# Optimization experiments

Measured on AMD Instinct MI355X. Metric: run time of the kernel, lower is better.

Reference implementation:

```python
import jax, jax.numpy as jnp
import numpy as np

N_NODES = 100000
N_EDGES = 1600000
IN_CH, HID_CH, OUT_CH = 128, 256, 128


def _sage_conv(x, src, dst, W_l, b_l, W_r, n_nodes):
    """PyG SAGEConv with mean aggregation: lin_l(mean_j x_j) + lin_r(x)."""
    # gather source features per edge, scatter-sum into destination nodes
    agg = jax.ops.segment_sum(x[src], dst, num_segments=n_nodes)  # [N, C]
    deg = jax.ops.segment_sum(jnp.ones((src.shape[0],), x.dtype), dst,
                              num_segments=n_nodes)               # [N]
    mean = agg / jnp.maximum(deg, 1.0)[:, None]
    return mean @ W_l + b_l + x @ W_r


def setup_inputs() -> dict:
    key = jax.random.key(0)
    ks = jax.random.split(key, 8)
    x = jax.random.normal(ks[0], (N_NODES, IN_CH), dtype=jnp.float32)
    edge_index = jax.random.randint(ks[1], (2, N_EDGES), 0, N_NODES, dtype=jnp.int64)
    s1 = 1.0 / np.sqrt(IN_CH)
    s2 = 1.0 / np.sqrt(HID_CH)
    W1_l = jax.random.normal(ks[2], (IN_CH, HID_CH), dtype=jnp.float32) * s1
    W1_r = jax.random.normal(ks[3], (IN_CH, HID_CH), dtype=jnp.float32) * s1
    b1 = jnp.zeros((HID_CH,), dtype=jnp.float32)
    W2_l = jax.random.normal(ks[4], (HID_CH, OUT_CH), dtype=jnp.float32) * s2
    W2_r = jax.random.normal(ks[5], (HID_CH, OUT_CH), dtype=jnp.float32) * s2
    b2 = jnp.zeros((OUT_CH,), dtype=jnp.float32)
    return {"x": x, "edge_index": edge_index, "W1_l": W1_l, "b1": b1,
            "W1_r": W1_r, "W2_l": W2_l, "b2": b2, "W2_r": W2_r}


def reference(x, edge_index, W1_l, b1, W1_r, W2_l, b2, W2_r):
    src, dst = edge_index[0], edge_index[1]
    h = _sage_conv(x, src, dst, W1_l, b1, W1_r, N_NODES)
    h = jax.nn.relu(h)
    out = _sage_conv(h, src, dst, W2_l, b2, W2_r, N_NODES)
    return out
```

## Files before the change

kernel.cpp:

```cpp
#include <hip/hip_runtime.h>
#include <cstddef>

#define N_NODES_C 100000
#define N_EDGES_C 1600000

#define NPB 64
#define NB 1563
#define SENT_ROW 100000

#define NCB 196
#define K2_EPB 8192
#define K2_BLOCKS 196

#define CONV_BLOCKS 12500
#define WB_BLOCKS 512

typedef unsigned short u16;
typedef __attribute__((ext_vector_type(8))) short bf16x8;
typedef __attribute__((ext_vector_type(4))) float f32x4;

__device__ __forceinline__ u16 f2bf(float f) {
    unsigned u = __float_as_uint(f);
    u += 0x7fffu + ((u >> 16) & 1);
    return (u16)(u >> 16);
}
__device__ __forceinline__ float lo16f(unsigned v) {
    return __uint_as_float(v << 16);
}
__device__ __forceinline__ float hi16f(unsigned v) {
    return __uint_as_float(v & 0xffff0000u);
}


__global__ __launch_bounds__(256) void front_fused(
    const float* __restrict__ x,
    const float* __restrict__ W1l, const float* __restrict__ W1r,
    const float* __restrict__ W2l, const float* __restrict__ W2r,
    u16* __restrict__ x_bf, u16* __restrict__ T1l, u16* __restrict__ T1r,
    u16* __restrict__ T2l, u16* __restrict__ T2r, u16* __restrict__ p2z) {
    const int b = blockIdx.x;
    const int t = threadIdx.x;
    if (b < CONV_BLOCKS) {
        int i = b * 256 + t;
        if (i < 3200000) {
            float4 v = ((const float4*)x)[i];
            ushort4 o;
            o.x = f2bf(v.x); o.y = f2bf(v.y); o.z = f2bf(v.z); o.w = f2bf(v.w);
            ((ushort4*)x_bf)[i] = o;
        }
    } else if (b < CONV_BLOCKS + WB_BLOCKS) {
        int id = (b - CONV_BLOCKS) * 256 + t;
        int which = id >> 15;
        int r = id & 32767;
        if (which == 0) {
            int n = r >> 7, k = r & 127;
            T1l[r] = f2bf(W1l[k * 256 + n]);
        } else if (which == 1) {
            int n = r >> 7, k = r & 127;
            T1r[r] = f2bf(W1r[k * 256 + n]);
        } else if (which == 2) {
            int n = r >> 8, k = r & 255;
            T2l[r] = f2bf(W2l[k * 128 + n]);
        } else {
            int n = r >> 8, k = r & 255;
            T2r[r] = f2bf(W2r[k * 128 + n]);
        }
    } else {
        uint4 z; z.x = 0; z.y = 0; z.z = 0; z.w = 0;
        if (t < 16)
            ((uint4*)(x_bf + (size_t)SENT_ROW * 128))[t] = z;
        else if (t < 32)
            ((uint4*)(p2z + (size_t)SENT_ROW * 128))[t - 16] = z;
    }
}


__global__ __launch_bounds__(1024) void hist196(const int* __restrict__ dst,
                                                int* __restrict__ chist) {
    __shared__ int hist[NCB];
    const int t = threadIdx.x;
    if (t < NCB) hist[t] = 0;
    __syncthreads();
    const int e0 = blockIdx.x * K2_EPB;
#pragma unroll
    for (int r = 0; r < 2; ++r) {
        int i = (e0 >> 2) + r * 1024 + t;
        if (i * 4 < N_EDGES_C) {
            int4 d = ((const int4*)dst)[i];
            atomicAdd(&hist[d.x >> 9], 1);
            atomicAdd(&hist[d.y >> 9], 1);
            atomicAdd(&hist[d.z >> 9], 1);
            atomicAdd(&hist[d.w >> 9], 1);
        }
    }
    __syncthreads();
    if (t < NCB) {
        int c = hist[t];
        if (c) atomicAdd(&chist[t], c);
    }
}


__global__ __launch_bounds__(256) void cscan(const int* __restrict__ chist,
                                             int* __restrict__ cbase,
                                             int* __restrict__ ccursor) {
    __shared__ int s[256];
    int t = threadIdx.x;
    int v = (t < NCB) ? chist[t] : 0;
    s[t] = v;
    __syncthreads();
    for (int off = 1; off < 256; off <<= 1) {
        int u = (t >= off) ? s[t - off] : 0;
        __syncthreads();
        s[t] += u;
        __syncthreads();
    }
    if (t < NCB) {
        int e = s[t] - v;
        cbase[t] = e;
        ccursor[t] = e;
    }
}


__global__ __launch_bounds__(1024) void coarse_scatter(
    const int* __restrict__ src, const int* __restrict__ dst,
    int* __restrict__ ccursor, unsigned* __restrict__ epkt2) {
    __shared__ unsigned spkt[K2_EPB];
    __shared__ unsigned char scb[K2_EPB];
    __shared__ int hist[NCB], lstart[NCB], lcur[NCB], grun[NCB], stmp[NCB];

    const int t = threadIdx.x;
    const int e0 = blockIdx.x * K2_EPB;
    const int cnt = min(K2_EPB, N_EDGES_C - e0);

    if (t < NCB) hist[t] = 0;
    __syncthreads();

    int4 dd[2], ss[2];
    int vi[2];
#pragma unroll
    for (int r = 0; r < 2; ++r) {
        int i = (e0 >> 2) + r * 1024 + t;
        vi[r] = (i * 4 < N_EDGES_C);
        if (vi[r]) {
            dd[r] = ((const int4*)dst)[i];
            ss[r] = ((const int4*)src)[i];
            atomicAdd(&hist[dd[r].x >> 9], 1);
            atomicAdd(&hist[dd[r].y >> 9], 1);
            atomicAdd(&hist[dd[r].z >> 9], 1);
            atomicAdd(&hist[dd[r].w >> 9], 1);
        }
    }
    __syncthreads();

    if (t < NCB) stmp[t] = hist[t];
    __syncthreads();
    for (int off = 1; off < NCB; off <<= 1) {
        int v = 0;
        if (t < NCB && t >= off) v = stmp[t - off];
        __syncthreads();
        if (t < NCB) stmp[t] += v;
        __syncthreads();
    }
    if (t < NCB) {
        int excl = stmp[t] - hist[t];
        lstart[t] = excl;
        lcur[t] = excl;
        if (hist[t]) grun[t] = atomicAdd(&ccursor[t], hist[t]);
    }
    __syncthreads();

#pragma unroll
    for (int r = 0; r < 2; ++r) {
        if (vi[r]) {
            int4 d = dd[r];
            int4 s4 = ss[r];
            {
                int cb = d.x >> 9;
                int pos = atomicAdd(&lcur[cb], 1);
                spkt[pos] = ((unsigned)(d.x & 511) << 17) | (unsigned)s4.x;
                scb[pos] = (unsigned char)cb;
            }
            {
                int cb = d.y >> 9;
                int pos = atomicAdd(&lcur[cb], 1);
                spkt[pos] = ((unsigned)(d.y & 511) << 17) | (unsigned)s4.y;
                scb[pos] = (unsigned char)cb;
            }
            {
                int cb = d.z >> 9;
                int pos = atomicAdd(&lcur[cb], 1);
                spkt[pos] = ((unsigned)(d.z & 511) << 17) | (unsigned)s4.z;
                scb[pos] = (unsigned char)cb;
            }
            {
                int cb = d.w >> 9;
                int pos = atomicAdd(&lcur[cb], 1);
                spkt[pos] = ((unsigned)(d.w & 511) << 17) | (unsigned)s4.w;
                scb[pos] = (unsigned char)cb;
            }
        }
    }
    __syncthreads();

#pragma unroll
    for (int k = 0; k < K2_EPB / 1024; ++k) {
        int i = k * 1024 + t;
        if (i < cnt) {
            int cb = scb[i];
            epkt2[grun[cb] + (i - lstart[cb])] = spkt[i];
        }
    }
}


__global__ __launch_bounds__(1024) void fine_sort(
    const int* __restrict__ cbase, const int* __restrict__ chist,
    const unsigned* __restrict__ epkt2, unsigned* __restrict__ esrc,
    int* __restrict__ deg, int* __restrict__ base) {
    __shared__ int hist[512], lstart[512], lcur[512], stmp[512];
    const int t = threadIdx.x;
    const int c = blockIdx.x;
    const int s0 = cbase[c];
    const int cnt = chist[c];

    if (t < 512) hist[t] = 0;
    __syncthreads();

    for (int i = t; i < cnt; i += 1024)
        atomicAdd(&hist[epkt2[s0 + i] >> 17], 1);
    __syncthreads();

    if (t < 512) stmp[t] = hist[t];
    __syncthreads();
    for (int off = 1; off < 512; off <<= 1) {
        int v = 0;
        if (t < 512 && t >= off) v = stmp[t - off];
        __syncthreads();
        if (t < 512) stmp[t] += v;
        __syncthreads();
    }
    if (t < 512) {
        int excl = stmp[t] - hist[t];
        lstart[t] = excl;
        lcur[t] = excl;
        int node = c * 512 + t;
        if (node < N_NODES_C) {
            deg[node] = hist[t];
            base[node] = s0 + excl;
        }
    }
    __syncthreads();

    for (int i = t; i < cnt; i += 1024) {
        unsigned p = epkt2[s0 + i];
        int pos = atomicAdd(&lcur[p >> 17], 1);
        esrc[s0 + pos] = p & 0x1ffffu;
    }
}


__global__ __launch_bounds__(512, 6) void fused_gemm_agg(
    const u16* __restrict__ x_bf, const int* __restrict__ deg,
    const int* __restrict__ base, const unsigned* __restrict__ esrc,
    const u16* __restrict__ T1l, const u16* __restrict__ T1r,
    const u16* __restrict__ T2l, const u16* __restrict__ T2r,
    const float* __restrict__ b1, const float* __restrict__ b2,
    u16* __restrict__ p2, u16* __restrict__ outp, int M) {
    alignas(16) __shared__ u16 uni[64 * 256];
    alignas(16) __shared__ u16 Bs[8192];

    u16* const meanS = uni;
    u16* const xS = uni + 64 * 128;
    u16* const hfrag = uni;

    const int tid = threadIdx.x;
    const int lane = tid & 63;
    const int wave = tid >> 6;
    const int qm = lane & 15;
    const int quad = lane >> 4;
    const int b = blockIdx.x;
    const int m0 = b * 64;

#pragma unroll
    for (int r = 0; r < 2; ++r) {
        int c = r * 512 + tid;
        int row = c >> 4, q16 = c & 15;
        __builtin_amdgcn_global_load_lds(
            (const __attribute__((address_space(1))) unsigned*)(
                x_bf + (size_t)(m0 + row) * 128 + ((q16 ^ (row & 7)) * 8)),
            (__attribute__((address_space(3))) unsigned*)(xS + c * 8), 16, 0, 0);
    }

    const int li8 = qm * 8;
    const int gbase = lane & 48;

    for (int pass = 0; pass < 2; ++pass) {
        int n = pass * 32 + wave * 4 + quad;
        int node = m0 + n;
        int d = 0, s0 = 0;
        if (node < N_NODES_C) { d = deg[node]; s0 = base[node]; }
        int dmax = max(d, __shfl_xor(d, 16, 64));
        dmax = max(dmax, __shfl_xor(dmax, 32, 64));

        float a0 = 0.f, a1 = 0.f, a2 = 0.f, a3 = 0.f;
        float a4 = 0.f, a5 = 0.f, a6 = 0.f, a7 = 0.f;

        for (int j = 0; j < dmax; j += 16) {
            int jj = j + qm;
            unsigned sidx = (jj < d) ? esrc[s0 + jj] : (unsigned)SENT_ROW;
            for (int u = 0; u < 16 && j + u < dmax; u += 4) {
                unsigned i0 = __shfl(sidx, gbase + u, 64);
                unsigned i1 = __shfl(sidx, gbase + u + 1, 64);
                unsigned i2 = __shfl(sidx, gbase + u + 2, 64);
                unsigned i3 = __shfl(sidx, gbase + u + 3, 64);
                uint4 r0 = *(const uint4*)(x_bf + (size_t)i0 * 128 + li8);
                uint4 r1 = *(const uint4*)(x_bf + (size_t)i1 * 128 + li8);
                uint4 r2 = *(const uint4*)(x_bf + (size_t)i2 * 128 + li8);
                uint4 r3 = *(const uint4*)(x_bf + (size_t)i3 * 128 + li8);
                a0 += lo16f(r0.x); a1 += hi16f(r0.x);
                a2 += lo16f(r0.y); a3 += hi16f(r0.y);
                a4 += lo16f(r0.z); a5 += hi16f(r0.z);
                a6 += lo16f(r0.w); a7 += hi16f(r0.w);
                a0 += lo16f(r1.x); a1 += hi16f(r1.x);
                a2 += lo16f(r1.y); a3 += hi16f(r1.y);
                a4 += lo16f(r1.z); a5 += hi16f(r1.z);
                a6 += lo16f(r1.w); a7 += hi16f(r1.w);
                a0 += lo16f(r2.x); a1 += hi16f(r2.x);
                a2 += lo16f(r2.y); a3 += hi16f(r2.y);
                a4 += lo16f(r2.z); a5 += hi16f(r2.z);
                a6 += lo16f(r2.w); a7 += hi16f(r2.w);
                a0 += lo16f(r3.x); a1 += hi16f(r3.x);
                a2 += lo16f(r3.y); a3 += hi16f(r3.y);
                a4 += lo16f(r3.z); a5 += hi16f(r3.z);
                a6 += lo16f(r3.w); a7 += hi16f(r3.w);
            }
        }

        float inv = d > 0 ? 1.f / (float)d : 0.f;
        uint4 o;
        o.x = (unsigned)f2bf(a0 * inv) | ((unsigned)f2bf(a1 * inv) << 16);
        o.y = (unsigned)f2bf(a2 * inv) | ((unsigned)f2bf(a3 * inv) << 16);
        o.z = (unsigned)f2bf(a4 * inv) | ((unsigned)f2bf(a5 * inv) << 16);
        o.w = (unsigned)f2bf(a6 * inv) | ((unsigned)f2bf(a7 * inv) << 16);
        *(uint4*)(meanS + n * 128 + ((qm ^ (n & 7)) * 8)) = o;
    }
    __syncthreads();

    const int wr0 = (wave >> 1) * 16;
    const int wc0 = (wave & 1) * 128;
    f32x4 acch[8];
#pragma unroll
    for (int j = 0; j < 8; ++j) acch[j] = (f32x4){0.f, 0.f, 0.f, 0.f};

#pragma unroll
    for (int mat = 0; mat < 2; ++mat) {
        const u16* __restrict__ W = mat ? T1r : T1l;
        const u16* Al = mat ? xS : meanS;
#pragma unroll
        for (int k0 = 0; k0 < 128; k0 += 32) {
#pragma unroll
            for (int r = 0; r < 2; ++r) {
                int c = r * 512 + tid;
                int row = c >> 2, kc = c & 3;
                __builtin_amdgcn_global_load_lds(
                    (const __attribute__((address_space(1))) unsigned*)(
                        W + (size_t)row * 128 + k0 + ((kc ^ (row & 3)) * 8)),
                    (__attribute__((address_space(3))) unsigned*)(Bs + c * 8), 16, 0, 0);
            }
            __syncthreads();
            int ch0 = k0 >> 3;
            int rowA = wr0 + qm;
            bf16x8 af = *(const bf16x8*)(Al + rowA * 128 +
                                         (((ch0 + quad) ^ (rowA & 7)) * 8));
            bf16x8 bfv[8];
#pragma unroll
            for (int j = 0; j < 8; ++j) {
                int rB = wc0 + j * 16 + qm;
                bfv[j] = *(const bf16x8*)(Bs + rB * 32 + ((quad ^ (rB & 3)) * 8));
            }
#pragma unroll
            for (int j = 0; j < 8; ++j)
                acch[j] = __builtin_amdgcn_mfma_f32_16x16x32_bf16(af, bfv[j],
                                                                  acch[j], 0, 0, 0);
            __syncthreads();
        }
    }

#pragma unroll
    for (int j = 0; j < 8; ++j) {
        int n = wc0 + j * 16 + qm;
        float bb = b1[n];
        int ks = n >> 5, quadB = (n >> 3) & 3, jB = n & 7;
#pragma unroll
        for (int r = 0; r < 4; ++r) {
            int mloc = wr0 + quad * 4 + r;
            float v = fmaxf(acch[j][r] + bb, 0.f);
            hfrag[((ks * 4 + (mloc >> 4)) * 16 + (mloc & 15)) * 32 + quadB * 8 + jB] =
                f2bf(v);
        }
    }
    __syncthreads();

    const int wrB = (wave >> 1) * 16;
    const int wcB = (wave & 1) * 64;
    f32x4 accp[4], acco[4];
#pragma unroll
    for (int j = 0; j < 4; ++j) {
        accp[j] = (f32x4){0.f, 0.f, 0.f, 0.f};
        acco[j] = (f32x4){0.f, 0.f, 0.f, 0.f};
    }

#pragma unroll
    for (int ks = 0; ks < 8; ++ks) {
#pragma unroll
        for (int r = 0; r < 2; ++r) {
            int c = r * 512 + tid;
            int matc = c >> 9;
            int row = (c >> 2) & 127;
            int kc = c & 3;
            const u16* W = matc ? T2r : T2l;
            __builtin_amdgcn_global_load_lds(
                (const __attribute__((address_space(1))) unsigned*)(
                    W + (size_t)row * 256 + ks * 32 + ((kc ^ (row & 3)) * 8)),
                (__attribute__((address_space(3))) unsigned*)(Bs + c * 8), 16, 0, 0);
        }
        __syncthreads();
        bf16x8 af = *(const bf16x8*)(hfrag +
                                     ((ks * 4 + (wrB >> 4)) * 16 + qm) * 32 + quad * 8);
        bf16x8 bfl[4], bfr[4];
#pragma unroll
        for (int j = 0; j < 4; ++j) {
            int rB = wcB + j * 16 + qm;
            bfl[j] = *(const bf16x8*)(Bs + rB * 32 + ((quad ^ (rB & 3)) * 8));
            bfr[j] = *(const bf16x8*)(Bs + 4096 + rB * 32 + ((quad ^ (rB & 3)) * 8));
        }
#pragma unroll
        for (int j = 0; j < 4; ++j) {
            accp[j] = __builtin_amdgcn_mfma_f32_16x16x32_bf16(af, bfl[j],
                                                              accp[j], 0, 0, 0);
            acco[j] = __builtin_amdgcn_mfma_f32_16x16x32_bf16(af, bfr[j],
                                                              acco[j], 0, 0, 0);
        }
        __syncthreads();
    }

#pragma unroll
    for (int j = 0; j < 4; ++j) {
        int n = wcB + j * 16 + qm;
        float bb2 = b2[n];
#pragma unroll
        for (int r = 0; r < 4; ++r) {
            int row = m0 + wrB + quad * 4 + r;
            if (row < M) {
                p2[(size_t)row * 128 + n] = f2bf(accp[j][r]);
                outp[(size_t)row * 128 + n] = f2bf(acco[j][r] + bb2);
            }
        }
    }
}


__global__ __launch_bounds__(256, 8) void agg_final(const u16* __restrict__ tbl,
                                                    const int* __restrict__ deg,
                                                    const int* __restrict__ base,
                                                    const unsigned* __restrict__ esrc,
                                                    const u16* __restrict__ resid,
                                                    float* __restrict__ outv) {
    const int t = threadIdx.x;
    const int wave = t >> 6;
    const int lane = t & 63;
    const int qm = lane & 15;
    const int quad = lane >> 4;
    const int b = blockIdx.x;
    const int li8 = qm * 8;
    const int gbase = lane & 48;

    for (int pass = 0; pass < 4; ++pass) {
        int n = pass * 16 + wave * 4 + quad;
        int node = b * NPB + n;
        bool valid = node < N_NODES_C;
        int d = 0, s0 = 0;
        if (valid) { d = deg[node]; s0 = base[node]; }
        int dmax = max(d, __shfl_xor(d, 16, 64));
        dmax = max(dmax, __shfl_xor(dmax, 32, 64));

        float a0 = 0.f, a1 = 0.f, a2 = 0.f, a3 = 0.f;
        float a4 = 0.f, a5 = 0.f, a6 = 0.f, a7 = 0.f;

        for (int j = 0; j < dmax; j += 16) {
            int jj = j + qm;
            unsigned sidx = (jj < d) ? esrc[s0 + jj] : (unsigned)SENT_ROW;
            for (int u = 0; u < 16 && j + u < dmax; u += 4) {
                unsigned i0 = __shfl(sidx, gbase + u, 64);
                unsigned i1 = __shfl(sidx, gbase + u + 1, 64);
                unsigned i2 = __shfl(sidx, gbase + u + 2, 64);
                unsigned i3 = __shfl(sidx, gbase + u + 3, 64);
                uint4 r0 = *(const uint4*)(tbl + (size_t)i0 * 128 + li8);
                uint4 r1 = *(const uint4*)(tbl + (size_t)i1 * 128 + li8);
                uint4 r2 = *(const uint4*)(tbl + (size_t)i2 * 128 + li8);
                uint4 r3 = *(const uint4*)(tbl + (size_t)i3 * 128 + li8);
                a0 += lo16f(r0.x); a1 += hi16f(r0.x);
                a2 += lo16f(r0.y); a3 += hi16f(r0.y);
                a4 += lo16f(r0.z); a5 += hi16f(r0.z);
                a6 += lo16f(r0.w); a7 += hi16f(r0.w);
                a0 += lo16f(r1.x); a1 += hi16f(r1.x);
                a2 += lo16f(r1.y); a3 += hi16f(r1.y);
                a4 += lo16f(r1.z); a5 += hi16f(r1.z);
                a6 += lo16f(r1.w); a7 += hi16f(r1.w);
                a0 += lo16f(r2.x); a1 += hi16f(r2.x);
                a2 += lo16f(r2.y); a3 += hi16f(r2.y);
                a4 += lo16f(r2.z); a5 += hi16f(r2.z);
                a6 += lo16f(r2.w); a7 += hi16f(r2.w);
                a0 += lo16f(r3.x); a1 += hi16f(r3.x);
                a2 += lo16f(r3.y); a3 += hi16f(r3.y);
                a4 += lo16f(r3.z); a5 += hi16f(r3.z);
                a6 += lo16f(r3.w); a7 += hi16f(r3.w);
            }
        }

        if (valid) {
            float inv = d > 0 ? 1.f / (float)d : 0.f;
            uint4 rp = *(const uint4*)(resid + (size_t)node * 128 + li8);
            float* op = outv + (size_t)node * 128 + li8;
            float4 o0, o1;
            o0.x = a0 * inv + lo16f(rp.x);
            o0.y = a1 * inv + hi16f(rp.x);
            o0.z = a2 * inv + lo16f(rp.y);
            o0.w = a3 * inv + hi16f(rp.y);
            o1.x = a4 * inv + lo16f(rp.z);
            o1.y = a5 * inv + hi16f(rp.z);
            o1.z = a6 * inv + lo16f(rp.w);
            o1.w = a7 * inv + hi16f(rp.w);
            *(float4*)op = o0;
            *(float4*)(op + 4) = o1;
        }
    }
}


extern "C" void kernel_launch(void* const* d_in, const int* in_sizes, int n_in,
                              void* d_out, int out_size, void* d_ws, size_t ws_size,
                              hipStream_t stream) {
    const float* x = (const float*)d_in[0];
    const int* ei = (const int*)d_in[1];
    const float* W1l = (const float*)d_in[2];
    const float* b1 = (const float*)d_in[3];
    const float* W1r = (const float*)d_in[4];
    const float* W2l = (const float*)d_in[5];
    const float* b2 = (const float*)d_in[6];
    const float* W2r = (const float*)d_in[7];
    float* out = (float*)d_out;

    const int* src = ei;
    const int* dst = ei + N_EDGES_C;

    int* iw = (int*)d_ws;
    int* chist = iw;
    int* cbase = iw + 256;
    int* ccursor = iw + 512;
    int* deg = iw + 768;
    int* base = iw + 100768;
    unsigned* epkt2 = (unsigned*)(iw + 200768);
    unsigned* esrc = (unsigned*)(iw + 1800768);
    u16* T1l = (u16*)(iw + 3400832);
    u16* T1r = T1l + 32768;
    u16* T2l = T1r + 32768;
    u16* T2r = T2l + 32768;
    u16* ub = (u16*)((char*)d_ws + (16u << 20));
    u16* x_bf = ub;
    u16* p2 = ub + 12850000;
    u16* outp = ub + 25700000;

    hipMemsetAsync(chist, 0, 1024, stream);

    front_fused<<<CONV_BLOCKS + WB_BLOCKS + 1, 256, 0, stream>>>(
        x, W1l, W1r, W2l, W2r, x_bf, T1l, T1r, T2l, T2r, p2);
    hist196<<<K2_BLOCKS, 1024, 0, stream>>>(dst, chist);
    cscan<<<1, 256, 0, stream>>>(chist, cbase, ccursor);
    coarse_scatter<<<K2_BLOCKS, 1024, 0, stream>>>(src, dst, ccursor, epkt2);
    fine_sort<<<NCB, 1024, 0, stream>>>(cbase, chist, epkt2, esrc, deg, base);

    fused_gemm_agg<<<NB, 512, 0, stream>>>(x_bf, deg, base, esrc, T1l, T1r, T2l,
                                           T2r, b1, b2, p2, outp, N_NODES_C);
    agg_final<<<NB, 256, 0, stream>>>(p2, deg, base, esrc, outp, out);
}
```

Baseline: 343.5 us.

## Fuse histogram with weight prep and overlap x bf16 conversion with sort kernels

Merges the coarse histogram into the weight-transpose prep kernel, which drops one launch. The fp32-to-bf16 conversion of x moves out of the front kernel and is split across extra blocks appended to the coarse scatter and fine sort kernels. Those kernels leave the GPU underused with only 196 blocks, so the conversion can fill idle CUs. The risk is that the conversion blocks compete with the sort blocks for bandwidth and LDS occupancy, and the 1024-thread blocks for a streaming conversion may schedule less well.

Measured after the change: 337.3 us. No clear change (-1.8%).

```diff
diff --git a/kernel.cpp b/kernel.cpp
--- a/kernel.cpp
+++ b/kernel.cpp
@@ -12,8 +12,8 @@
 #define K2_EPB 8192
 #define K2_BLOCKS 196
 
-#define CONV_BLOCKS 12500
-#define WB_BLOCKS 512
+#define CONV1_BLOCKS 1563
+#define CONV2_BLOCKS 1562
 
 typedef unsigned short u16;
 typedef __attribute__((ext_vector_type(8))) short bf16x8;
@@ -31,25 +31,47 @@
     return __uint_as_float(v & 0xffff0000u);
 }
 
-
-__global__ __launch_bounds__(256) void front_fused(
-    const float* __restrict__ x,
+__device__ __forceinline__ void conv_chunk(const float* __restrict__ x,
+                                           u16* __restrict__ x_bf, int i) {
+    float4 v = ((const float4*)x)[i];
+    ushort4 o;
+    o.x = f2bf(v.x); o.y = f2bf(v.y); o.z = f2bf(v.z); o.w = f2bf(v.w);
+    ((ushort4*)x_bf)[i] = o;
+}
+
+
+__global__ __launch_bounds__(1024) void prep_a(
+    const int* __restrict__ dst,
     const float* __restrict__ W1l, const float* __restrict__ W1r,
     const float* __restrict__ W2l, const float* __restrict__ W2r,
-    u16* __restrict__ x_bf, u16* __restrict__ T1l, u16* __restrict__ T1r,
-    u16* __restrict__ T2l, u16* __restrict__ T2r, u16* __restrict__ p2z) {
+    u16* __restrict__ T1l, u16* __restrict__ T1r,
+    u16* __restrict__ T2l, u16* __restrict__ T2r,
+    int* __restrict__ chist, u16* __restrict__ x_bf, u16* __restrict__ p2z) {
     const int b = blockIdx.x;
     const int t = threadIdx.x;
-    if (b < CONV_BLOCKS) {
-        int i = b * 256 + t;
-        if (i < 3200000) {
-            float4 v = ((const float4*)x)[i];
-            ushort4 o;
-            o.x = f2bf(v.x); o.y = f2bf(v.y); o.z = f2bf(v.z); o.w = f2bf(v.w);
-            ((ushort4*)x_bf)[i] = o;
-        }
-    } else if (b < CONV_BLOCKS + WB_BLOCKS) {
-        int id = (b - CONV_BLOCKS) * 256 + t;
+    if (b < K2_BLOCKS) {
+        __shared__ int hist[NCB];
+        if (t < NCB) hist[t] = 0;
+        __syncthreads();
+        const int e0 = b * K2_EPB;
+#pragma unroll
+        for (int r = 0; r < 2; ++r) {
+            int i = (e0 >> 2) + r * 1024 + t;
+            if (i * 4 < N_EDGES_C) {
+                int4 d = ((const int4*)dst)[i];
+                atomicAdd(&hist[d.x >> 9], 1);
+                atomicAdd(&hist[d.y >> 9], 1);
+                atomicAdd(&hist[d.z >> 9], 1);
+                atomicAdd(&hist[d.w >> 9], 1);
+            }
+        }
+        __syncthreads();
+        if (t < NCB) {
+            int c = hist[t];
+            if (c) atomicAdd(&chist[t], c);
+        }
+    } else if (b < K2_BLOCKS + 128) {
+        int id = (b - K2_BLOCKS) * 1024 + t;
         int which = id >> 15;
         int r = id & 32767;
         if (which == 0) {
@@ -75,32 +97,6 @@
 }
 
 
-__global__ __launch_bounds__(1024) void hist196(const int* __restrict__ dst,
-                                                int* __restrict__ chist) {
-    __shared__ int hist[NCB];
-    const int t = threadIdx.x;
-    if (t < NCB) hist[t] = 0;
-    __syncthreads();
-    const int e0 = blockIdx.x * K2_EPB;
-#pragma unroll
-    for (int r = 0; r < 2; ++r) {
-        int i = (e0 >> 2) + r * 1024 + t;
-        if (i * 4 < N_EDGES_C) {
-            int4 d = ((const int4*)dst)[i];
-            atomicAdd(&hist[d.x >> 9], 1);
-            atomicAdd(&hist[d.y >> 9], 1);
-            atomicAdd(&hist[d.z >> 9], 1);
-            atomicAdd(&hist[d.w >> 9], 1);
-        }
-    }
-    __syncthreads();
-    if (t < NCB) {
-        int c = hist[t];
-        if (c) atomicAdd(&chist[t], c);
-    }
-}
-
-
 __global__ __launch_bounds__(256) void cscan(const int* __restrict__ chist,
                                              int* __restrict__ cbase,
                                              int* __restrict__ ccursor) {
@@ -123,15 +119,21 @@
 }
 
 
-__global__ __launch_bounds__(1024) void coarse_scatter(
+__global__ __launch_bounds__(1024) void scatter_conv(
     const int* __restrict__ src, const int* __restrict__ dst,
-    int* __restrict__ ccursor, unsigned* __restrict__ epkt2) {
+    int* __restrict__ ccursor, unsigned* __restrict__ epkt2,
+    const float* __restrict__ x, u16* __restrict__ x_bf) {
     __shared__ unsigned spkt[K2_EPB];
     __shared__ unsigned char scb[K2_EPB];
     __shared__ int hist[NCB], lstart[NCB], lcur[NCB], grun[NCB], stmp[NCB];
 
     const int t = threadIdx.x;
-    const int e0 = blockIdx.x * K2_EPB;
+    const int b = blockIdx.x;
+    if (b >= K2_BLOCKS) {
+        conv_chunk(x, x_bf, (b - K2_BLOCKS) * 1024 + t);
+        return;
+    }
+    const int e0 = b * K2_EPB;
     const int cnt = min(K2_EPB, N_EDGES_C - e0);
 
     if (t < NCB) hist[t] = 0;
@@ -215,13 +217,18 @@
 }
 
 
-__global__ __launch_bounds__(1024) void fine_sort(
+__global__ __launch_bounds__(1024) void sort_conv(
     const int* __restrict__ cbase, const int* __restrict__ chist,
     const unsigned* __restrict__ epkt2, unsigned* __restrict__ esrc,
-    int* __restrict__ deg, int* __restrict__ base) {
+    int* __restrict__ deg, int* __restrict__ base,
+    const float* __restrict__ x, u16* __restrict__ x_bf) {
     __shared__ int hist[512], lstart[512], lcur[512], stmp[512];
     const int t = threadIdx.x;
     const int c = blockIdx.x;
+    if (c >= K2_BLOCKS) {
+        conv_chunk(x, x_bf, 1600512 + (c - K2_BLOCKS) * 1024 + t);
+        return;
+    }
     const int s0 = cbase[c];
     const int cnt = chist[c];
 
@@ -575,12 +582,13 @@
 
     hipMemsetAsync(chist, 0, 1024, stream);
 
-    front_fused<<<CONV_BLOCKS + WB_BLOCKS + 1, 256, 0, stream>>>(
-        x, W1l, W1r, W2l, W2r, x_bf, T1l, T1r, T2l, T2r, p2);
-    hist196<<<K2_BLOCKS, 1024, 0, stream>>>(dst, chist);
+    prep_a<<<K2_BLOCKS + 128 + 1, 1024, 0, stream>>>(
+        dst, W1l, W1r, W2l, W2r, T1l, T1r, T2l, T2r, chist, x_bf, p2);
     cscan<<<1, 256, 0, stream>>>(chist, cbase, ccursor);
-    coarse_scatter<<<K2_BLOCKS, 1024, 0, stream>>>(src, dst, ccursor, epkt2);
-    fine_sort<<<NCB, 1024, 0, stream>>>(cbase, chist, epkt2, esrc, deg, base);
+    scatter_conv<<<K2_BLOCKS + CONV1_BLOCKS, 1024, 0, stream>>>(
+        src, dst, ccursor, epkt2, x, x_bf);
+    sort_conv<<<K2_BLOCKS + CONV2_BLOCKS, 1024, 0, stream>>>(
+        cbase, chist, epkt2, esrc, deg, base, x, x_bf);
 
     fused_gemm_agg<<<NB, 512, 0, stream>>>(x_bf, deg, base, esrc, T1l, T1r, T2l,
                                            T2r, b1, b2, p2, outp, N_NODES_C);
```
